# Optimization experiments

Hardware: AMD Instinct MI355X
Metric: run time of the kernel (lower is better)

The kernel has to match this reference:

```python
import jax, jax.numpy as jnp
import numpy as np
from jax import lax


def _l2n(t, eps=1e-12):
    n = jnp.sqrt(jnp.sum(t * t, axis=-1, keepdims=True))
    return t / jnp.maximum(n, eps)


def _ln(t, w, b, eps=1e-5):
    mu = jnp.mean(t, -1, keepdims=True)
    var = jnp.var(t, -1, keepdims=True)
    return (t - mu) / jnp.sqrt(var + eps) * w + b


def _unfold3(x):
    # nn.Unfold(kernel_size=3, padding=1, stride=1): [B,C,H,W] -> [B,C,9,H*W]
    B, C, H, W = x.shape
    xp = jnp.pad(x, ((0, 0), (0, 0), (1, 1), (1, 1)))
    pat = jnp.stack([xp[:, :, i:i + H, j:j + W] for i in range(3) for j in range(3)], axis=2)
    return pat.reshape(B, C, 9, H * W)


def _forward(x, norm1_w, norm1_b, q_w, q_b, kv_w, kv_b, temperature, query_embedding,
             learnable_tokens, learnable_bias, sr_w, sr_b, pln_w, pln_b, proj_w, proj_b,
             norm2_w, norm2_b, fc1_w, fc1_b, dw_w, dw_b, fc2_w, fc2_b):
    B, C, H, W = x.shape
    nh = temperature.shape[0]
    d = C // nh
    N = H * W
    K = 9  # local_len = window_size**2
    # norm1 (WithBias LayerNorm over channel dim, channels-last)
    y = _ln(x.reshape(B, C, N).transpose(0, 2, 1), norm1_w, norm1_b)  # [B,N,C]
    # ---- AggregatedAttention ----
    q = (y @ q_w.T + q_b).reshape(B, N, nh, d).transpose(0, 2, 1, 3)  # [B,h,N,d]
    qn = _l2n(q)
    qs = (qn + query_embedding) * jax.nn.softplus(temperature)
    kv = y @ kv_w.T + kv_b  # [B,N,2C]
    k_loc = _l2n(kv[..., :C].reshape(B, N, nh, d)).reshape(B, N, C)
    kvl = jnp.concatenate([k_loc, kv[..., C:]], -1).transpose(0, 2, 1).reshape(B, 2 * C, H, W)
    pat = _unfold3(kvl).reshape(B, 2 * nh, d, K, N).transpose(0, 1, 4, 2, 3)  # [B,2h,N,d,K]
    k_l, v_l = pat[:, :nh], pat[:, nh:]
    attn_local = jnp.einsum('bhnd,bhndk->bhnk', qs, k_l)  # [B,h,N,K]
    # pooled branch; sr_ratio=1 so adaptive_avg_pool2d is identity
    y4 = y.transpose(0, 2, 1).reshape(B, C, H, W)
    xp = jax.nn.gelu(jnp.einsum('oc,bchw->bohw', sr_w, y4) + sr_b[:, None, None], approximate=False)
    xp = _ln(xp.reshape(B, C, N).transpose(0, 2, 1), pln_w, pln_b)  # [B,pool_len,C]
    kvp = (xp @ kv_w.T + kv_b).reshape(B, N, 2 * nh, d).transpose(0, 2, 1, 3)
    k_p = _l2n(kvp[:, :nh])
    v_p = kvp[:, nh:]
    attn_pool = jnp.einsum('bhnd,bhmd->bhnm', qs, k_p)  # [B,h,N,pool_len]
    attn = jax.nn.softmax(jnp.concatenate([attn_local, attn_pool], -1), axis=-1)
    a_l, a_p = attn[..., :K], attn[..., K:]
    w_l = jnp.einsum('bhnd,hdk->bhnk', qn, learnable_tokens) + learnable_bias + a_l
    x_local = jnp.einsum('bhnk,bhndk->bhnd', w_l, v_l)
    x_pool = jnp.einsum('bhnm,bhmd->bhnd', a_p, v_p)
    xo = (x_local + x_pool).transpose(0, 2, 1, 3).reshape(B, N, C)
    # proj then raw torch-style reshape [B,N,C] -> [B,C,H,W] (memory reinterpretation)
    xo = (xo @ proj_w.T + proj_b).reshape(B, C, H, W)
    x = x + xo
    # ---- ConvolutionalGLU MLP ----
    hf = dw_b.shape[0]
    y2 = _ln(x.reshape(B, C, N).transpose(0, 2, 1), norm2_w, norm2_b).transpose(0, 2, 1).reshape(B, C, H, W)
    f1 = jnp.einsum('oc,bchw->bohw', fc1_w, y2) + fc1_b[:, None, None]
    a, v = f1[:, :hf], f1[:, hf:]
    dw = lax.conv_general_dilated(a, dw_w, (1, 1), ((1, 1), (1, 1)),
                                  feature_group_count=hf,
                                  dimension_numbers=('NCHW', 'OIHW', 'NCHW')) + dw_b[:, None, None]
    g = jax.nn.gelu(dw, approximate=False) * v
    out = jnp.einsum('oc,bchw->bohw', fc2_w, g) + fc2_b[:, None, None]
    return x + out


def setup_inputs() -> dict:
    key = jax.random.key(0)
    B, C, H, W = 2, 128, 56, 56
    nh, d, K = 4, 32, 9
    hf = int(2 * int(C * 4.0) / 3)  # 341
    ks = iter(jax.random.split(key, 16))
    rn = lambda shape, s=0.02: jax.random.normal(next(ks), shape, jnp.float32) * s
    return {
        'x': jax.random.normal(next(ks), (B, C, H, W), jnp.float32),
        'norm1_w': jnp.ones((C,), jnp.float32), 'norm1_b': jnp.zeros((C,), jnp.float32),
        'q_w': rn((C, C)), 'q_b': jnp.zeros((C,), jnp.float32),
        'kv_w': rn((2 * C, C)), 'kv_b': jnp.zeros((2 * C,), jnp.float32),
        'temperature': jnp.full((nh, 1, 1), float(np.log(np.exp(1.0 / 0.24) - 1.0)), jnp.float32),
        'query_embedding': rn((nh, 1, d)),
        'learnable_tokens': rn((nh, d, K)),
        'learnable_bias': jnp.zeros((nh, 1, K), jnp.float32),
        'sr_w': rn((C, C)), 'sr_b': jnp.zeros((C,), jnp.float32),
        'pln_w': jnp.ones((C,), jnp.float32), 'pln_b': jnp.zeros((C,), jnp.float32),
        'proj_w': rn((C, C)), 'proj_b': jnp.zeros((C,), jnp.float32),
        'norm2_w': jnp.ones((C,), jnp.float32), 'norm2_b': jnp.zeros((C,), jnp.float32),
        'fc1_w': rn((2 * hf, C)), 'fc1_b': jnp.zeros((2 * hf,), jnp.float32),
        'dw_w': rn((hf, 1, 3, 3)), 'dw_b': jnp.zeros((hf,), jnp.float32),
        'fc2_w': rn((C, hf)), 'fc2_b': jnp.zeros((C,), jnp.float32),
    }


def reference(x, norm1_w, norm1_b, q_w, q_b, kv_w, kv_b, temperature, query_embedding,
              learnable_tokens, learnable_bias, sr_w, sr_b, pln_w, pln_b, proj_w, proj_b,
              norm2_w, norm2_b, fc1_w, fc1_b, dw_w, dw_b, fc2_w, fc2_b):
    return _forward(x, norm1_w, norm1_b, q_w, q_b, kv_w, kv_b, temperature, query_embedding,
                    learnable_tokens, learnable_bias, sr_w, sr_b, pln_w, pln_b, proj_w, proj_b,
                    norm2_w, norm2_b, fc1_w, fc1_b, dw_w, dw_b, fc2_w, fc2_b)
```

## Files before the change

### kernel.cpp

```cpp
#include <hip/hip_runtime.h>
#include <hip/hip_bf16.h>

typedef __hip_bfloat16 bf16;
typedef _Float16 f16;
typedef short s8v __attribute__((ext_vector_type(8)));
typedef short s4v __attribute__((ext_vector_type(4)));
typedef float f4v __attribute__((ext_vector_type(4)));
typedef _Float16 h4v __attribute__((ext_vector_type(4)));

#define DEVI __device__ __forceinline__

DEVI float cvt(float x){ return x; }
DEVI float cvt(bf16 x){ return __bfloat162float(x); }

DEVI void stg(float* p, float v){ *p = v; }
DEVI void stg(bf16* p, float v){ *p = __float2bfloat16(v); }

DEVI float gelu_exact(float x){
  return 0.5f*x*(1.0f + erff(x*0.70710678118654752440f));
}

constexpr int B_ = 2, C_ = 128, H_ = 56, W_ = 56, N_ = 3136, NH_ = 4, D_ = 32, HF_ = 341;
constexpr int ROWS_ = B_*N_;
constexpr int KF2 = 352;
constexpr int GQ_ = NH_*B_*N_;
constexpr int FW = 512;
constexpr int KSP = 12;
constexpr int SPLIT = 256;
constexpr float LOG2E = 1.4426950408889634f;
constexpr float E8L2  = 11.541560327111707f;

template<typename TX, typename TY, bool PLANES>
__global__ __launch_bounds__(256)
void ln_kernel(const TX* __restrict__ x, long xstr, const float* __restrict__ w,
               const float* __restrict__ bia, TY* __restrict__ y)
{
  int gid = blockIdx.x*4 + (threadIdx.x>>6);
  int lane = threadIdx.x & 63;
  int b = gid / N_, n = gid % N_;
  float v0, v1;
  if (PLANES){
    v0 = cvt(x[((long)b*C_ + lane     )*N_ + n]);
    v1 = cvt(x[((long)b*C_ + lane + 64)*N_ + n]);
  } else {
    v0 = cvt(x[(long)gid*xstr + lane     ]);
    v1 = cvt(x[(long)gid*xstr + lane + 64]);
  }
  float s = v0+v1, ss = v0*v0 + v1*v1;
  #pragma unroll
  for (int o=32;o>0;o>>=1){ s += __shfl_xor(s,o); ss += __shfl_xor(ss,o); }
  float mu  = s*(1.0f/128.0f);
  float var = fmaxf(ss*(1.0f/128.0f) - mu*mu, 0.f);
  float inv = rsqrtf(var + 1e-5f);
  stg(&y[(long)gid*C_ + lane     ], (v0-mu)*inv*w[lane     ] + bia[lane     ]);
  stg(&y[(long)gid*C_ + lane + 64], (v1-mu)*inv*w[lane + 64] + bia[lane + 64]);
}

__global__ __launch_bounds__(256)
void convw_kernel(const float* __restrict__ q_w, const float* __restrict__ kv_w,
                  const float* __restrict__ sr_w, const float* __restrict__ proj_w,
                  const float* __restrict__ fc1_w, const float* __restrict__ fc2_w,
                  const float* __restrict__ q_b, const float* __restrict__ kv_b,
                  const float* __restrict__ sr_b,
                  bf16* __restrict__ out, float* __restrict__ bias_out)
{
  int t = blockIdx.x*256 + threadIdx.x;
  if (t >= 214272){
    int i = t - 214272;
    if (i < 512){
      float bv = (i < 128) ? q_b[i] : (i < 384) ? kv_b[i-128] : sr_b[i-384];
      bias_out[i] = bv;
    }
    return;
  }
  float v;
  if      (t <  16384) v = q_w[t];
  else if (t <  49152) v = kv_w[t-16384];
  else if (t <  65536) v = sr_w[t-49152];
  else if (t <  81920) v = proj_w[t-65536];
  else if (t < 169216) v = fc1_w[t-81920];
  else {
    int i = t - 169216; int m = i / KF2, kp = i % KF2;
    v = (kp < HF_) ? fc2_w[m*HF_ + kp] : 0.f;
  }
  out[t] = __float2bfloat16(v);
}

template<int KT, int MODE, typename TC>
__global__ __launch_bounds__(256)
void gemm_mfma(const bf16* __restrict__ A, const bf16* __restrict__ B,
               const float* __restrict__ bias, const float* __restrict__ res,
               TC* __restrict__ Cm, int M, int Nn,
               long sA, long sB, long sC, long sR,
               const float* __restrict__ qe, const float* __restrict__ temp,
               bf16* __restrict__ aux0, f16* __restrict__ aux1)
{
  A  += (long)blockIdx.z * sA;
  B  += (long)blockIdx.z * sB;
  Cm += (long)blockIdx.z * sC;
  if (res) res += (long)blockIdx.z * sR;
  int lane = threadIdx.x & 63, w = threadIdx.x >> 6;
  int m = lane & 15, quad = lane >> 4;
  int n0 = blockIdx.x*64, m0 = blockIdx.y*64;
  int arow = m0 + w*16 + m;
  if (arow >= M) arow = M-1;
  const bf16* ap = A + (long)arow*KT + quad*8;
  const bf16* bp = B + (long)(n0 + m)*KT + quad*8;
  f4v acc[4];
  #pragma unroll
  for (int s=0;s<4;s++) acc[s] = (f4v){0.f,0.f,0.f,0.f};
  #pragma unroll
  for (int k0 = 0; k0 < KT; k0 += 32){
    s8v af = *(const s8v*)(ap + k0);
    #pragma unroll
    for (int s=0;s<4;s++){
      s8v bf = *(const s8v*)(bp + (long)s*16*KT + k0);
      acc[s] = __builtin_amdgcn_mfma_f32_16x16x32_bf16(af, bf, acc[s], 0, 0, 0);
    }
  }
  if ((MODE==6 || MODE==7) && blockIdx.x < 2){
    int hA = blockIdx.x*2, hB = hA+1;
    float spA = 0.f, spB = 0.f;
    if (MODE==6){
      spA = log1pf(expf(temp[hA])) * LOG2E;
      spB = log1pf(expf(temp[hB])) * LOG2E;
    }
    #pragma unroll
    for (int r=0;r<4;r++){
      float v4[4];
      #pragma unroll
      for (int s=0;s<4;s++) v4[s] = acc[s][r] + bias[n0 + s*16 + m];
      float ssA = v4[0]*v4[0] + v4[1]*v4[1];
      float ssB = v4[2]*v4[2] + v4[3]*v4[3];
      #pragma unroll
      for (int off=1; off<16; off<<=1){
        ssA += __shfl_xor(ssA, off);
        ssB += __shfl_xor(ssB, off);
      }
      float invA = 1.f/fmaxf(sqrtf(ssA), 1e-12f);
      float invB = 1.f/fmaxf(sqrtf(ssB), 1e-12f);
      int gm = m0 + w*16 + quad*4 + r;
      int b = gm / N_, n = gm % N_;
      #pragma unroll
      for (int s=0;s<4;s++){
        int h = (s<2) ? hA : hB;
        int d = (s&1)*16 + m;
        float v = v4[s] * ((s<2) ? invA : invB);
        if (MODE==6) v = (v + qe[h*D_ + d]) * ((s<2) ? spA : spB);
        aux0[((long)(b*NH_+h)*N_ + n)*D_ + d] = __float2bfloat16(v);
      }
    }
    return;
  }
  if (MODE==7){
    int gm0 = m0 + w*16 + quad*4;
    int b = gm0 / N_, nb = gm0 % N_;
    #pragma unroll
    for (int s=0;s<4;s++){
      int h = (blockIdx.x-2)*2 + (s>>1);
      int d = (s&1)*16 + m;
      f16 p4[4];
      #pragma unroll
      for (int r=0;r<4;r++) p4[r] = (f16)(acc[s][r] + bias[n0 + s*16 + m]);
      *(s4v*)(aux1 + ((long)(b*NH_+h)*D_ + d)*N_ + nb) = *(const s4v*)p4;
    }
    return;
  }
  #pragma unroll
  for (int s=0;s<4;s++){
    int gn = n0 + s*16 + m;
    #pragma unroll
    for (int r=0;r<4;r++){
      int gm = m0 + w*16 + quad*4 + r;
      if (gm >= M) continue;
      float v = acc[s][r];
      if (MODE==1 || MODE==4 || MODE==6) v += bias[gn];
      else                               v += bias[gm];
      if (MODE==6 && gn >= 384) v = gelu_exact(v);
      if (MODE==4 || MODE==5) v += res[(long)gm*Nn + gn];
      stg(&Cm[(long)gm*Nn + gn], v);
    }
  }
}

__global__ __launch_bounds__(256)
void attn_part_kernel(const bf16* __restrict__ qs_, const bf16* __restrict__ kp_,
                      const f16* __restrict__ vp_,
                      bf16* __restrict__ Op, float* __restrict__ Lp)
{
  int bh = blockIdx.y;
  int z  = blockIdx.z;
  int lane = threadIdx.x & 63;
  int w    = threadIdx.x >> 6;
  int m    = lane & 15, quad = lane >> 4;
  int base = blockIdx.x*256 + w*16;
  __shared__ float sm[4][640];
  float* Olds = sm[w];

  s8v af[4]; bool hasQ[4];
  #pragma unroll
  for (int ch=0; ch<4; ch++){
    int qq = base + ch*64;
    hasQ[ch] = (qq < N_);
    af[ch] = *(const s8v*)(qs_ + ((long)bh*N_ + (hasQ[ch] ? qq : base) + m)*D_ + quad*8);
  }
  const bf16* kpb = kp_ + (long)bh*N_*D_;
  const f16*  vpb = vp_ + (long)bh*D_*N_;
  f4v o0[4], o1[4];
  float l[4];
  #pragma unroll
  for (int ch=0; ch<4; ch++){
    o0[ch] = (f4v){0.f,0.f,0.f,0.f}; o1[ch] = (f4v){0.f,0.f,0.f,0.f};
    l[ch] = 0.f;
  }

  int tlo = z*SPLIT, thi = (z==KSP-1) ? N_ : tlo + SPLIT;
  for (int t0 = tlo; t0 < thi; t0 += 64){
    s8v kf[4];
    #pragma unroll
    for (int s=0;s<4;s++)
      kf[s] = *(const s8v*)(kpb + (long)(t0 + s*16 + m)*D_ + quad*8);
    h4v vf0[4], vf1[4];
    #pragma unroll
    for (int s=0;s<4;s++){
      vf0[s] = *(const h4v*)(vpb + (long)(m     )*N_ + t0 + s*16 + quad*4);
      vf1[s] = *(const h4v*)(vpb + (long)(16 + m)*N_ + t0 + s*16 + quad*4);
    }
    #pragma unroll
    for (int s = 0; s < 4; s++){
      #pragma unroll
      for (int ch=0; ch<4; ch++){
        f4v c = {-E8L2, -E8L2, -E8L2, -E8L2};
        c = __builtin_amdgcn_mfma_f32_16x16x32_bf16(kf[s], af[ch], c, 0, 0, 0);
        float e0 = __builtin_amdgcn_exp2f(c[0]);
        float e1 = __builtin_amdgcn_exp2f(c[1]);
        float e2 = __builtin_amdgcn_exp2f(c[2]);
        float e3 = __builtin_amdgcn_exp2f(c[3]);
        l[ch] += (e0+e1) + (e2+e3);
        h4v p; p[0] = (f16)e0; p[1] = (f16)e1; p[2] = (f16)e2; p[3] = (f16)e3;
        o0[ch] = __builtin_amdgcn_mfma_f32_16x16x16f16(p, vf0[s], o0[ch], 0, 0, 0);
        o1[ch] = __builtin_amdgcn_mfma_f32_16x16x16f16(p, vf1[s], o1[ch], 0, 0, 0);
      }
    }
  }
  #pragma unroll
  for (int ch=0; ch<4; ch++){
    if (!hasQ[ch]) continue;
    float lr = l[ch];
    lr += __shfl_xor(lr, 16);
    lr += __shfl_xor(lr, 32);
    #pragma unroll
    for (int r=0;r<4;r++){
      Olds[(quad*4+r)*36 + m     ] = o0[ch][r];
      Olds[(quad*4+r)*36 + 16 + m] = o1[ch][r];
    }
    long gq = (long)bh*N_ + base + ch*64 + m;
    f4v ov0 = *(const f4v*)(Olds + m*36 + quad*8);
    f4v ov1 = *(const f4v*)(Olds + m*36 + quad*8 + 4);
    bf16 o8[8];
    #pragma unroll
    for (int j=0;j<4;j++){ o8[j] = __float2bfloat16(ov0[j]); o8[4+j] = __float2bfloat16(ov1[j]); }
    *(s8v*)(Op + ((long)z*GQ_ + gq)*32 + quad*8) = *(const s8v*)o8;
    if (quad == 0) Lp[(long)z*GQ_ + gq] = lr;
  }
}

__global__ __launch_bounds__(256)
void attn_combine_kernel(const bf16* __restrict__ Op, const float* __restrict__ Lp,
                         const bf16* __restrict__ qs_, const bf16* __restrict__ fused,
                         const float* __restrict__ qe, const float* __restrict__ temp,
                         const float* __restrict__ tokens, const float* __restrict__ tbias,
                         bf16* __restrict__ xo)
{
  int t  = blockIdx.x*256 + threadIdx.x;
  int gq = t >> 3;
  int l8 = t & 7;
  int d0 = l8*4;
  int n = gq % N_; int bh = gq / N_; int h = bh & 3; int b = bh >> 2;
  float out[4] = {0.f,0.f,0.f,0.f};
  #pragma unroll
  for (int z=0; z<KSP; z++){
    s4v o4 = *(const s4v*)(Op + ((long)z*GQ_ + gq)*32 + d0);
    #pragma unroll
    for (int j=0;j<4;j++) out[j] += cvt(((const bf16*)&o4)[j]);
  }
  float L = 0.f;
  for (int z=l8; z<KSP; z+=8) L += Lp[(long)z*GQ_ + gq];
  #pragma unroll
  for (int off=1; off<8; off<<=1) L += __shfl_xor(L, off);
  float q[4];
  {
    s4v q4 = *(const s4v*)(qs_ + (long)gq*D_ + d0);
    #pragma unroll
    for (int j=0;j<4;j++) q[j] = cvt(((const bf16*)&q4)[j]) * 0.6931471805599453f;
  }
  int hy = n / W_, wx = n % W_;
  const bf16* kvb = fused + (long)b*N_*FW + 128 + h*D_ + d0;
  float sl[9];
  #pragma unroll
  for (int k=0;k<9;k++){
    int di = k/3-1, dj = k%3-1;
    int yy = hy+di, xx = wx+dj;
    bool ok = (yy>=0 && yy<H_ && xx>=0 && xx<W_);
    float dot = 0.f, ss = 0.f;
    if (ok){
      s4v k4 = *(const s4v*)(kvb + (long)(yy*W_+xx)*FW);
      #pragma unroll
      for (int j=0;j<4;j++){
        float kk = cvt(((const bf16*)&k4)[j]);
        dot = fmaf(q[j], kk, dot);
        ss  = fmaf(kk, kk, ss);
      }
    }
    #pragma unroll
    for (int off=1; off<8; off<<=1){
      dot += __shfl_xor(dot, off);
      ss  += __shfl_xor(ss,  off);
    }
    sl[k] = ok ? dot / fmaxf(sqrtf(ss), 1e-12f) : 0.f;
  }
  #pragma unroll
  for (int k=0;k<9;k++) L += __expf(sl[k] - 8.f);
  float invL = 1.f/L;
  #pragma unroll
  for (int j=0;j<4;j++) out[j] *= invL;
  float sp = log1pf(expf(temp[h]));
  float invsp = 1.f/sp;
  float qn[4];
  #pragma unroll
  for (int j=0;j<4;j++) qn[j] = q[j]*invsp - qe[h*D_ + d0 + j];
  #pragma unroll
  for (int k=0;k<9;k++){
    float tok = 0.f;
    #pragma unroll
    for (int j=0;j<4;j++) tok = fmaf(qn[j], tokens[(h*D_ + d0 + j)*9 + k], tok);
    #pragma unroll
    for (int off=1; off<8; off<<=1) tok += __shfl_xor(tok, off);
    float wl = tok + tbias[h*9+k] + __expf(sl[k] - 8.f)*invL;
    int di = k/3-1, dj = k%3-1;
    int yy = hy+di, xx = wx+dj;
    if (yy>=0 && yy<H_ && xx>=0 && xx<W_){
      s4v v4 = *(const s4v*)(kvb + (long)(yy*W_+xx)*FW + 128);
      #pragma unroll
      for (int j=0;j<4;j++) out[j] = fmaf(wl, cvt(((const bf16*)&v4)[j]), out[j]);
    }
  }
  bf16 o4[4];
  #pragma unroll
  for (int j=0;j<4;j++) o4[j] = __float2bfloat16(out[j]);
  *(s4v*)(xo + ((long)(b*N_ + n))*C_ + h*D_ + d0) = *(const s4v*)o4;
}

__global__ __launch_bounds__(256)
void dwconv_kernel(const bf16* __restrict__ f1, const float* __restrict__ dww,
                   const float* __restrict__ dwb, bf16* __restrict__ g)
{
  int t = blockIdx.x*256 + threadIdx.x;
  if (t >= B_*N_*44) return;
  int b = t / (N_*44); int r = t - b*(N_*44);
  int n = r % N_, cg = r / N_;
  f1 += (long)b*2*HF_*N_;
  g  += (long)b*N_*KF2;
  int c0 = cg*8;
  int hy = n / W_, wx = n % W_;
  bf16 o8[8];
  #pragma unroll
  for (int j=0;j<8;j++){
    int c = c0 + j;
    float val = 0.f;
    if (c < HF_){
      const bf16* ap = f1 + (long)c*N_;
      float s = dwb[c];
      #pragma unroll
      for (int di=-1; di<=1; di++)
        #pragma unroll
        for (int dj=-1; dj<=1; dj++){
          int yy = hy+di, xx = wx+dj;
          if (yy>=0 && yy<H_ && xx>=0 && xx<W_)
            s = fmaf(dww[c*9 + (di+1)*3 + (dj+1)], cvt(ap[yy*W_+xx]), s);
        }
      val = gelu_exact(s) * cvt(f1[(long)(HF_+c)*N_ + n]);
    }
    o8[j] = __float2bfloat16(val);
  }
  *(s8v*)(g + (long)n*KF2 + c0) = *(const s8v*)o8;
}

extern "C" void kernel_launch(void* const* d_in, const int* in_sizes, int n_in,
                              void* d_out, int out_size, void* d_ws, size_t ws_size,
                              hipStream_t stream)
{
  (void)in_sizes; (void)n_in; (void)out_size; (void)ws_size;
  const float* x_in      = (const float*)d_in[0];
  const float* norm1_w   = (const float*)d_in[1];
  const float* norm1_b   = (const float*)d_in[2];
  const float* q_w       = (const float*)d_in[3];
  const float* q_b       = (const float*)d_in[4];
  const float* kv_w      = (const float*)d_in[5];
  const float* kv_b      = (const float*)d_in[6];
  const float* temp      = (const float*)d_in[7];
  const float* qe        = (const float*)d_in[8];
  const float* tokens    = (const float*)d_in[9];
  const float* tbias     = (const float*)d_in[10];
  const float* sr_w      = (const float*)d_in[11];
  const float* sr_b      = (const float*)d_in[12];
  const float* pln_w     = (const float*)d_in[13];
  const float* pln_b     = (const float*)d_in[14];
  const float* proj_w    = (const float*)d_in[15];
  const float* proj_b    = (const float*)d_in[16];
  const float* norm2_w   = (const float*)d_in[17];
  const float* norm2_b   = (const float*)d_in[18];
  const float* fc1_w     = (const float*)d_in[19];
  const float* fc1_b     = (const float*)d_in[20];
  const float* dw_w      = (const float*)d_in[21];
  const float* dw_b      = (const float*)d_in[22];
  const float* fc2_w     = (const float*)d_in[23];
  const float* fc2_b     = (const float*)d_in[24];

  char* w8 = (char*)d_ws;
  bf16*  fused   = (bf16*)(w8 + 0);
  float* x2      = (float*)(w8 + 0);
  bf16*  y2      = (bf16*)(w8 + 3211264);
  bf16*  f1b     = (bf16*)(w8 + 4816896);
  bf16*  qs      = (bf16*)(w8 + 6422528);
  bf16*  xp      = (bf16*)(w8 + 8028160);
  bf16*  k_p     = (bf16*)(w8 + 9633792);
  f16*   v_p     = (f16*) (w8 + 11239424);
  bf16*  Opart   = (bf16*)(w8 + 13045056);
  bf16*  g_rows  = (bf16*)(w8 + 32312640);
  bf16*  wbase   = (bf16*)(w8 + 36728128);
  float* fbias   = (float*)(w8 + 37156672);
  bf16*  y       = f1b;
  bf16*  xo      = (bf16*)d_out;
  float* Lpart   = (float*)((char*)d_out + 1605632);
  bf16*  proj_wb = wbase + 65536;
  bf16*  fc1_wb  = wbase + 81920;
  bf16*  fc2_wb  = wbase + 169216;

  convw_kernel<<<(214784+255)/256, 256, 0, stream>>>(
      q_w, kv_w, sr_w, proj_w, fc1_w, fc2_w, q_b, kv_b, sr_b, wbase, fbias);
  ln_kernel<float, bf16, true><<<ROWS_/4, 256, 0, stream>>>(x_in, 0, norm1_w, norm1_b, y);
  gemm_mfma<128, 6, bf16><<<dim3(8,98), 256, 0, stream>>>(
      y, wbase, fbias, nullptr, fused, ROWS_, FW, 0,0,0,0, qe, temp, qs, nullptr);
  ln_kernel<bf16, bf16, false><<<ROWS_/4, 256, 0, stream>>>(fused + 384, FW, pln_w, pln_b, xp);
  gemm_mfma<128, 7, bf16><<<dim3(4,98), 256, 0, stream>>>(
      xp, wbase + 16384, kv_b, nullptr, (bf16*)nullptr, ROWS_, 256, 0,0,0,0,
      nullptr, nullptr, k_p, v_p);
  attn_part_kernel<<<dim3(13,8,KSP), 256, 0, stream>>>(qs, k_p, v_p, Opart, Lpart);
  attn_combine_kernel<<<GQ_*8/256, 256, 0, stream>>>(Opart, Lpart, qs, fused,
                                                     qe, temp, tokens, tbias, xo);
  gemm_mfma<128, 4, float><<<dim3(2,98), 256, 0, stream>>>(
      xo, proj_wb, proj_b, x_in, x2, ROWS_, 128, 0,0,0,0, nullptr, nullptr, nullptr, nullptr);
  ln_kernel<float, bf16, true><<<ROWS_/4, 256, 0, stream>>>(x2, 0, norm2_w, norm2_b, y2);
  gemm_mfma<128, 3, bf16><<<dim3(49,11,B_), 256, 0, stream>>>(
      fc1_wb, y2, fc1_b, nullptr, f1b, 2*HF_, N_,
      0, (long)N_*C_, (long)2*HF_*N_, 0, nullptr, nullptr, nullptr, nullptr);
  dwconv_kernel<<<(B_*N_*44+255)/256, 256, 0, stream>>>(f1b, dw_w, dw_b, g_rows);
  gemm_mfma<KF2, 5, float><<<dim3(49,2,B_), 256, 0, stream>>>(
      fc2_wb, g_rows, fc2_b, x2, (float*)d_out, C_, N_,
      0, (long)N_*KF2, (long)C_*N_, (long)C_*N_, nullptr, nullptr, nullptr, nullptr);
}
```

Measured before the change: 254.2 us.

## Fuse weight conversion with norm1, retune attention split and shrink GEMM M-tiles

Merges the weight-conversion kernel and the first LayerNorm into one launch, picking the path from the block index. Changes the attention key split from 12 chunks of 256 to 8 chunks of 384. Gives the proj and fc2 GEMMs a 32-row M tile with 128-thread blocks and twice as many blocks, to put more work in flight on the narrow-output GEMMs. Fewer split partitions means less combine work but less parallelism in the attention partial kernel.

```diff
diff --git a/kernel.cpp b/kernel.cpp
--- a/kernel.cpp
+++ b/kernel.cpp
@@ -25,8 +25,8 @@
 constexpr int KF2 = 352;
 constexpr int GQ_ = NH_*B_*N_;
 constexpr int FW = 512;
-constexpr int KSP = 12;
-constexpr int SPLIT = 256;
+constexpr int KSP = 8;
+constexpr int SPLIT = 384;
 constexpr float LOG2E = 1.4426950408889634f;
 constexpr float E8L2  = 11.541560327111707f;
 
@@ -57,13 +57,31 @@
 }
 
 __global__ __launch_bounds__(256)
-void convw_kernel(const float* __restrict__ q_w, const float* __restrict__ kv_w,
-                  const float* __restrict__ sr_w, const float* __restrict__ proj_w,
-                  const float* __restrict__ fc1_w, const float* __restrict__ fc2_w,
-                  const float* __restrict__ q_b, const float* __restrict__ kv_b,
-                  const float* __restrict__ sr_b,
-                  bf16* __restrict__ out, float* __restrict__ bias_out)
-{
+void head_kernel(const float* __restrict__ q_w, const float* __restrict__ kv_w,
+                 const float* __restrict__ sr_w, const float* __restrict__ proj_w,
+                 const float* __restrict__ fc1_w, const float* __restrict__ fc2_w,
+                 const float* __restrict__ q_b, const float* __restrict__ kv_b,
+                 const float* __restrict__ sr_b,
+                 bf16* __restrict__ out, float* __restrict__ bias_out,
+                 const float* __restrict__ x_in, const float* __restrict__ n1w,
+                 const float* __restrict__ n1b, bf16* __restrict__ y)
+{
+  if (blockIdx.x >= 839){
+    int gid = (blockIdx.x - 839)*4 + (threadIdx.x>>6);
+    int lane = threadIdx.x & 63;
+    int b = gid / N_, n = gid % N_;
+    float v0 = x_in[((long)b*C_ + lane     )*N_ + n];
+    float v1 = x_in[((long)b*C_ + lane + 64)*N_ + n];
+    float s = v0+v1, ss = v0*v0 + v1*v1;
+    #pragma unroll
+    for (int o=32;o>0;o>>=1){ s += __shfl_xor(s,o); ss += __shfl_xor(ss,o); }
+    float mu  = s*(1.0f/128.0f);
+    float var = fmaxf(ss*(1.0f/128.0f) - mu*mu, 0.f);
+    float inv = rsqrtf(var + 1e-5f);
+    y[(long)gid*C_ + lane     ] = __float2bfloat16((v0-mu)*inv*n1w[lane     ] + n1b[lane     ]);
+    y[(long)gid*C_ + lane + 64] = __float2bfloat16((v1-mu)*inv*n1w[lane + 64] + n1b[lane + 64]);
+    return;
+  }
   int t = blockIdx.x*256 + threadIdx.x;
   if (t >= 214272){
     int i = t - 214272;
@@ -86,7 +104,7 @@
   out[t] = __float2bfloat16(v);
 }
 
-template<int KT, int MODE, typename TC>
+template<int KT, int MODE, typename TC, int BM=64>
 __global__ __launch_bounds__(256)
 void gemm_mfma(const bf16* __restrict__ A, const bf16* __restrict__ B,
                const float* __restrict__ bias, const float* __restrict__ res,
@@ -101,7 +119,7 @@
   if (res) res += (long)blockIdx.z * sR;
   int lane = threadIdx.x & 63, w = threadIdx.x >> 6;
   int m = lane & 15, quad = lane >> 4;
-  int n0 = blockIdx.x*64, m0 = blockIdx.y*64;
+  int n0 = blockIdx.x*64, m0 = blockIdx.y*BM;
   int arow = m0 + w*16 + m;
   if (arow >= M) arow = M-1;
   const bf16* ap = A + (long)arow*KT + quad*8;
@@ -437,9 +455,9 @@
   bf16*  fc1_wb  = wbase + 81920;
   bf16*  fc2_wb  = wbase + 169216;
 
-  convw_kernel<<<(214784+255)/256, 256, 0, stream>>>(
-      q_w, kv_w, sr_w, proj_w, fc1_w, fc2_w, q_b, kv_b, sr_b, wbase, fbias);
-  ln_kernel<float, bf16, true><<<ROWS_/4, 256, 0, stream>>>(x_in, 0, norm1_w, norm1_b, y);
+  head_kernel<<<839 + ROWS_/4, 256, 0, stream>>>(
+      q_w, kv_w, sr_w, proj_w, fc1_w, fc2_w, q_b, kv_b, sr_b, wbase, fbias,
+      x_in, norm1_w, norm1_b, y);
   gemm_mfma<128, 6, bf16><<<dim3(8,98), 256, 0, stream>>>(
       y, wbase, fbias, nullptr, fused, ROWS_, FW, 0,0,0,0, qe, temp, qs, nullptr);
   ln_kernel<bf16, bf16, false><<<ROWS_/4, 256, 0, stream>>>(fused + 384, FW, pln_w, pln_b, xp);
@@ -449,14 +467,14 @@
   attn_part_kernel<<<dim3(13,8,KSP), 256, 0, stream>>>(qs, k_p, v_p, Opart, Lpart);
   attn_combine_kernel<<<GQ_*8/256, 256, 0, stream>>>(Opart, Lpart, qs, fused,
                                                      qe, temp, tokens, tbias, xo);
-  gemm_mfma<128, 4, float><<<dim3(2,98), 256, 0, stream>>>(
+  gemm_mfma<128, 4, float, 32><<<dim3(2,196), 128, 0, stream>>>(
       xo, proj_wb, proj_b, x_in, x2, ROWS_, 128, 0,0,0,0, nullptr, nullptr, nullptr, nullptr);
   ln_kernel<float, bf16, true><<<ROWS_/4, 256, 0, stream>>>(x2, 0, norm2_w, norm2_b, y2);
   gemm_mfma<128, 3, bf16><<<dim3(49,11,B_), 256, 0, stream>>>(
       fc1_wb, y2, fc1_b, nullptr, f1b, 2*HF_, N_,
       0, (long)N_*C_, (long)2*HF_*N_, 0, nullptr, nullptr, nullptr, nullptr);
   dwconv_kernel<<<(B_*N_*44+255)/256, 256, 0, stream>>>(f1b, dw_w, dw_b, g_rows);
-  gemm_mfma<KF2, 5, float><<<dim3(49,2,B_), 256, 0, stream>>>(
+  gemm_mfma<KF2, 5, float, 32><<<dim3(49,4,B_), 128, 0, stream>>>(
       fc2_wb, g_rows, fc2_b, x2, (float*)d_out, C_, N_,
       0, (long)N_*KF2, (long)C_*N_, (long)C_*N_, nullptr, nullptr, nullptr, nullptr);
 }
```

Result: no change. 253.8 us (-0.1%).
